# Performance work log

Measured on AMD Instinct MI355X. Metric: run time of the kernel, lower is better.

Reference implementation:

```python
import jax, jax.numpy as jnp
import numpy as np
from math import sqrt

P = 1.0  # axis-aligned transform exponent (init arg p)
EPS = 1e-6


def setup_inputs() -> dict:
    key = jax.random.key(0)
    k1, k2, k3, k4 = jax.random.split(key, 4)
    B, L, S, H, E = 4, 2048, 2048, 8, 64
    return {
        "queries": jax.random.normal(k1, (B, L, H, E), dtype=jnp.float32),
        "keys": jax.random.normal(k2, (B, S, H, E), dtype=jnp.float32),
        "values": jax.random.normal(k3, (B, S, H, E), dtype=jnp.float32),
        "attn_mask": jnp.zeros((1, 1, 1, 1), dtype=bool),  # unused: mask_flag=False
        "directional_weights": jnp.ones((1, 1, 1, 1), dtype=jnp.float32),
        "dynamic_param": jax.random.normal(k4, (1,), dtype=jnp.float32),
    }


def _transform(x, directional_weights, dynamic_param):
    # axis_aligned_transformation: rescale by (1/std over seq dim)^p (unbiased std, like torch)
    std = jnp.std(x, axis=-2, keepdims=True, ddof=1)
    x = x * (1.0 / (std + EPS)) ** P
    # directional_reweighting then nonlinear_mapping
    x = x * directional_weights
    return jnp.tanh(x) * dynamic_param


def reference(queries, keys, values, attn_mask, directional_weights, dynamic_param):
    B, L, H, E = queries.shape
    scale = 1.0 / sqrt(E)
    qt = _transform(queries, directional_weights, dynamic_param)  # [B,L,H,E]
    kt = _transform(keys, directional_weights, dynamic_param)     # [B,S,H,E]
    scores = jnp.einsum('blhe,bshe->bhls', qt, kt)                # [B,H,L,S]
    # per-row tau = sqrt(var(scores) + eps), unbiased variance like torch.var
    tau = jnp.sqrt(jnp.var(scores, axis=-1, keepdims=True, ddof=1) + EPS)
    A = jax.nn.softmax(scale * scores / tau, axis=-1)             # [B,H,L,S]
    V = jnp.einsum('bhls,bshd->blhd', A, values)                  # [B,L,H,D]
    return V
```

## Files before the change

kernel.cpp:

```cpp
#include <hip/hip_runtime.h>
#include <math.h>

#define B_ 4
#define L_ 2048
#define S_ 2048
#define H_ 8
#define E_ 64
#define BH_ (B_*H_)
#define EPS 1e-6f
#define LOG2E 1.44269504088896340736f

typedef __attribute__((ext_vector_type(8))) short short8;
typedef __attribute__((ext_vector_type(4))) float f32x4;

__device__ __forceinline__ unsigned short f2bf(float f) {
    unsigned int u = __float_as_uint(f);
    u = (u + 0x7fffu + ((u >> 16) & 1u)) >> 16;
    return (unsigned short)u;
}

__device__ __forceinline__ float bf2f(unsigned short u) {
    return __uint_as_float(((unsigned int)u) << 16);
}

__device__ __forceinline__ float fast_tanh(float x) {
    float e = __expf(2.0f * x);
    return 1.0f - 2.0f / (e + 1.0f);
}

__device__ __forceinline__ unsigned int cvt_pk_bf16(float lo, float hi) {
    unsigned int r;
    asm("v_cvt_pk_bf16_f32 %0, %1, %2" : "=v"(r) : "v"(lo), "v"(hi));
    return r;
}
__device__ __forceinline__ float exp2_fast(float x) {
    float r;
    asm("v_exp_f32 %0, %1" : "=v"(r) : "v"(x));
    return r;
}
__device__ __forceinline__ void swap32(unsigned int &a, unsigned int &b) {
    asm("v_permlane32_swap_b32 %0, %1" : "+v"(a), "+v"(b));
}
__device__ __forceinline__ void swap16(unsigned int &a, unsigned int &b) {
    asm("v_permlane16_swap_b32 %0, %1" : "+v"(a), "+v"(b));
}

__global__ __launch_bounds__(256) void pre_kernel(
    const float* __restrict__ xq, const float* __restrict__ xk,
    const float* __restrict__ xv,
    unsigned short* __restrict__ qt, unsigned short* __restrict__ kt,
    unsigned short* __restrict__ vt, float* __restrict__ Gf,
    const float* __restrict__ dwp, const float* __restrict__ dpp)
{
    __shared__ float ls[64][65];
    int bx = blockIdx.x;
    int tid = threadIdx.x;
    if (bx < 4096) {
        const float* x = (bx < 2048) ? xq : xk;
        unsigned short* xt = (bx < 2048) ? qt : kt;
        int wv = tid >> 6, ln = tid & 63;
        int bl = (bx & 2047) * 4 + wv;
        int b = bl >> 11, l = bl & 2047;
        const float* xb = x + (size_t)bl * 512;
        float4 fa = *(const float4*)(xb + ln * 4);
        float4 fb = *(const float4*)(xb + 256 + ln * 4);
        float s0 = fa.x + fb.x, s1 = fa.y + fb.y, s2 = fa.z + fb.z, s3 = fa.w + fb.w;
        float q0 = fa.x * fa.x + fb.x * fb.x, q1 = fa.y * fa.y + fb.y * fb.y;
        float q2 = fa.z * fa.z + fb.z * fb.z, q3 = fa.w * fa.w + fb.w * fb.w;
        s0 += __shfl_xor(s0, 16); s1 += __shfl_xor(s1, 16);
        s2 += __shfl_xor(s2, 16); s3 += __shfl_xor(s3, 16);
        q0 += __shfl_xor(q0, 16); q1 += __shfl_xor(q1, 16);
        q2 += __shfl_xor(q2, 16); q3 += __shfl_xor(q3, 16);
        s0 += __shfl_xor(s0, 32); s1 += __shfl_xor(s1, 32);
        s2 += __shfl_xor(s2, 32); s3 += __shfl_xor(s3, 32);
        q0 += __shfl_xor(q0, 32); q1 += __shfl_xor(q1, 32);
        q2 += __shfl_xor(q2, 32); q3 += __shfl_xor(q3, 32);
        float dw = dwp[0], d = dpp[0];
        auto mkw = [&](float s, float q) {
            float mean = s * 0.125f;
            float var = (q - s * mean) * (1.f / 7.f);
            var = fmaxf(var, 0.f);
            return dw / (sqrtf(var) + EPS);
        };
        float w0 = mkw(s0, q0), w1 = mkw(s1, q1), w2 = mkw(s2, q2), w3 = mkw(s3, q3);
        float ta0 = fast_tanh(fa.x * w0) * d, ta1 = fast_tanh(fa.y * w1) * d;
        float ta2 = fast_tanh(fa.z * w2) * d, ta3 = fast_tanh(fa.w * w3) * d;
        float tb0 = fast_tanh(fb.x * w0) * d, tb1 = fast_tanh(fb.y * w1) * d;
        float tb2 = fast_tanh(fb.z * w2) * d, tb3 = fast_tanh(fb.w * w3) * d;
        uint2 pa, pb;
        pa.x = cvt_pk_bf16(ta0, ta1); pa.y = cvt_pk_bf16(ta2, ta3);
        pb.x = cvt_pk_bf16(tb0, tb1); pb.y = cvt_pk_bf16(tb2, tb3);
        int hh = ln >> 4, e0 = (ln & 15) * 4;
        *(uint2*)(xt + ((size_t)(b * 8 + hh) * 2048 + l) * 64 + e0) = pa;
        *(uint2*)(xt + ((size_t)(b * 8 + hh + 4) * 2048 + l) * 64 + e0) = pb;
    } else if (bx < 5120) {
        int t2 = bx - 4096;
        int s0 = (t2 & 31) * 64;
        int h = (t2 >> 5) & 7, b = t2 >> 8;
        int t = tid;
#pragma unroll
        for (int i = 0; i < 4; ++i) {
            int idx = t + i * 256;
            int r = idx >> 4, c4 = (idx & 15) * 4;
            const float4 f = *(const float4*)&xv[((size_t)(b * S_ + s0 + r) * H_ + h) * E_ + c4];
            ls[r][c4] = f.x; ls[r][c4 + 1] = f.y; ls[r][c4 + 2] = f.z; ls[r][c4 + 3] = f.w;
        }
        __syncthreads();
        size_t ob = ((size_t)(b * H_ + h) * (S_ / 64) + (s0 >> 6)) * 4096;
#pragma unroll
        for (int i = 0; i < 2; ++i) {
            int ri = t + i * 256;
            int et = ri >> 7, c = (ri >> 6) & 1, quad = (ri >> 4) & 3, m = ri & 15;
            int e = et * 16 + m, sb = c * 32 + quad * 8;
            uint4 u;
            u.x = cvt_pk_bf16(ls[sb + 0][e], ls[sb + 1][e]);
            u.y = cvt_pk_bf16(ls[sb + 2][e], ls[sb + 3][e]);
            u.z = cvt_pk_bf16(ls[sb + 4][e], ls[sb + 5][e]);
            u.w = cvt_pk_bf16(ls[sb + 6][e], ls[sb + 7][e]);
            *(uint4*)&vt[ob + (size_t)ri * 8] = u;
        }
    } else {
        for (int i = (bx - 5120) * 256 + tid; i < 32 * 4096 + 32 * 64; i += 32 * 256)
            Gf[i] = 0.f;
    }
}

__global__ __launch_bounds__(256) void gram_kernel(
    unsigned short* __restrict__ kt, float* __restrict__ Gf,
    float* __restrict__ ksum)
{
    __shared__ unsigned short ks[128 * 72];
    __shared__ float gs[4096];
    int g2 = blockIdx.x;
    int bh = g2 >> 2, part = g2 & 3;
    unsigned short* base = kt + (size_t)bh * S_ * E_ + (size_t)part * 512 * E_;
    int tid = threadIdx.x, lane = tid & 63, w = tid >> 6;
    int m = lane & 15, quad = lane >> 4;

    f32x4 acc[4][4];
#pragma unroll
    for (int i = 0; i < 4; ++i)
#pragma unroll
        for (int j = 0; j < 4; ++j) acc[i][j] = (f32x4){0.f, 0.f, 0.f, 0.f};
    float ksp[4] = {0.f, 0.f, 0.f, 0.f};

    short8 stg[4];
#pragma unroll
    for (int i = 0; i < 4; ++i)
        stg[i] = *(const short8*)(base + (size_t)(tid + i * 256) * 8);

    for (int ch = 0; ch < 4; ++ch) {
        __syncthreads();
#pragma unroll
        for (int i = 0; i < 4; ++i) {
            int u = tid + i * 256;
            *(short8*)&ks[(u >> 3) * 72 + (u & 7) * 8] = stg[i];
        }
        __syncthreads();
        if (ch < 3) {
#pragma unroll
            for (int i = 0; i < 4; ++i)
                stg[i] = *(const short8*)(base + (size_t)(ch + 1) * 8192 + (tid + i * 256) * 8);
        }
#pragma unroll
        for (int tt = 0; tt < 2; ++tt)
#pragma unroll
            for (int i = 0; i < 2; ++i) {
                int u = tid + i * 256;
                int nt = u >> 7, cc = (u >> 6) & 1, ln2 = u & 63;
                int mm = ln2 & 15, qq = ln2 >> 4;
                short8 vv = *(const short8*)&ks[(tt * 64 + nt * 16 + mm) * 72 + cc * 32 + qq * 8];
                *(uint4*)&base[(size_t)(ch * 2 + tt) * 4096 + (size_t)u * 8] = *(uint4*)&vv;
            }
        int s0 = w * 32;
        short8 af[4];
#pragma unroll
        for (int i = 0; i < 4; ++i) {
            short8 a;
#pragma unroll
            for (int kk = 0; kk < 8; ++kk) {
                unsigned short uv = ks[(s0 + quad * 8 + kk) * 72 + i * 16 + m];
                a[kk] = (short)uv;
                ksp[i] += bf2f(uv);
            }
            af[i] = a;
        }
#pragma unroll
        for (int i = 0; i < 4; ++i)
#pragma unroll
            for (int j = 0; j < 4; ++j)
                acc[i][j] = __builtin_amdgcn_mfma_f32_16x16x32_bf16(af[i], af[j], acc[i][j], 0, 0, 0);
    }
#pragma unroll
    for (int i = 0; i < 4; ++i) {
        ksp[i] += __shfl_xor(ksp[i], 16);
        ksp[i] += __shfl_xor(ksp[i], 32);
    }
    if (lane < 16) {
#pragma unroll
        for (int i = 0; i < 4; ++i)
            atomicAdd(&ksum[bh * 64 + i * 16 + lane], ksp[i]);
    }
    for (int w2 = 0; w2 < 4; ++w2) {
        if (w == w2) {
#pragma unroll
            for (int i = 0; i < 4; ++i)
#pragma unroll
                for (int j = 0; j < 4; ++j)
#pragma unroll
                    for (int r = 0; r < 4; ++r) {
                        int idx = (i * 16 + quad * 4 + r) * 64 + j * 16 + m;
                        if (w2 == 0) gs[idx] = acc[i][j][r]; else gs[idx] += acc[i][j][r];
                    }
        }
        __syncthreads();
    }
#pragma unroll
    for (int ii = 0; ii < 16; ++ii) {
        int idx = tid + ii * 256;
        atomicAdd(&Gf[bh * 4096 + idx], gs[idx]);
    }
}

__global__ __launch_bounds__(256, 2) void attn_kernel(
    const unsigned short* __restrict__ qt,
    const unsigned short* __restrict__ ktf,
    const unsigned short* __restrict__ vt,
    const float* __restrict__ Gf,
    const float* __restrict__ ksum,
    float* __restrict__ out)
{
    __shared__ float2 ascr_s[4 * 32];
    const int tid = threadIdx.x;
    const int lane = tid & 63;
    const int w = tid >> 6;
    const int m = lane & 15;
    const int quad = lane >> 4;
    float2* ascr = ascr_s + w * 32;

    int blk = blockIdx.x;
    int bh = (blk & 7) * 4 + ((blk >> 3) & 3);
    int l0 = (blk >> 5) * 128;
    int b = bh >> 3, h = bh & 7;

    const unsigned short* qtb = qt + (size_t)bh * L_ * E_;
    const unsigned short* kb  = ktf + (size_t)bh * S_ * E_;
    const unsigned short* vtb = vt + (size_t)bh * (S_ / 64) * 4096;

    short8 qf[2][2];
#pragma unroll
    for (int g = 0; g < 2; ++g)
#pragma unroll
        for (int c = 0; c < 2; ++c)
            qf[g][c] = *(const short8*)(qtb + (size_t)(l0 + w * 32 + g * 16 + m) * E_ + c * 32 + quad * 8);

    float al2[2], nalm2[2];
    {
        const float* gb = Gf + (size_t)bh * 4096;
        short8 gfr[4][2];
#pragma unroll
        for (int j = 0; j < 4; ++j)
#pragma unroll
            for (int c = 0; c < 2; ++c) {
                const float* gp = gb + (size_t)(j * 16 + m) * 64 + c * 32 + quad * 8;
                float4 f0 = *(const float4*)gp;
                float4 f1 = *(const float4*)(gp + 4);
                uint4 u;
                u.x = cvt_pk_bf16(f0.x, f0.y); u.y = cvt_pk_bf16(f0.z, f0.w);
                u.z = cvt_pk_bf16(f1.x, f1.y); u.w = cvt_pk_bf16(f1.z, f1.w);
                gfr[j][c] = *(short8*)&u;
            }
        float ksl[4];
#pragma unroll
        for (int j = 0; j < 4; ++j) ksl[j] = ksum[bh * 64 + j * 16 + m];
#pragma unroll
        for (int g = 0; g < 2; ++g) {
            f32x4 accj[4];
#pragma unroll
            for (int j = 0; j < 4; ++j) {
                accj[j] = (f32x4){0.f, 0.f, 0.f, 0.f};
                accj[j] = __builtin_amdgcn_mfma_f32_16x16x32_bf16(qf[g][0], gfr[j][0], accj[j], 0, 0, 0);
                accj[j] = __builtin_amdgcn_mfma_f32_16x16x32_bf16(qf[g][1], gfr[j][1], accj[j], 0, 0, 0);
            }
            float ps[4] = {0, 0, 0, 0}, pr[4] = {0, 0, 0, 0};
#pragma unroll
            for (int r = 0; r < 4; ++r)
#pragma unroll
                for (int j = 0; j < 4; ++j) {
                    float qv = bf2f(qtb[(size_t)(l0 + w * 32 + g * 16 + quad * 4 + r) * E_ + j * 16 + m]);
                    ps[r] = fmaf(accj[j][r], qv, ps[r]);
                    pr[r] = fmaf(qv, ksl[j], pr[r]);
                }
#pragma unroll
            for (int mask = 1; mask < 16; mask <<= 1)
#pragma unroll
                for (int r = 0; r < 4; ++r) {
                    ps[r] += __shfl_xor(ps[r], mask);
                    pr[r] += __shfl_xor(pr[r], mask);
                }
            if (m == 0) {
#pragma unroll
                for (int r = 0; r < 4; ++r) {
                    float sum = pr[r];
                    float mu = sum * (1.f / S_);
                    float var = (ps[r] - sum * mu) * (1.f / (S_ - 1));
                    var = fmaxf(var, 0.f);
                    float tau = sqrtf(var + EPS);
                    float a = 0.125f / tau;
                    ascr[g * 16 + quad * 4 + r] = make_float2(a, a * mu);
                }
            }
        }
#pragma unroll
        for (int g = 0; g < 2; ++g) {
            float2 a2 = ascr[g * 16 + m];
            al2[g] = a2.x * LOG2E; nalm2[g] = -a2.y * LOG2E;
        }
    }

    f32x4 oacc[2][4];
#pragma unroll
    for (int g = 0; g < 2; ++g)
#pragma unroll
        for (int et = 0; et < 4; ++et) oacc[g][et] = (f32x4){0.f, 0.f, 0.f, 0.f};
    f32x4 asum2[2];
#pragma unroll
    for (int g = 0; g < 2; ++g) asum2[g] = (f32x4){0.f, 0.f, 0.f, 0.f};

    short8 ones;
#pragma unroll
    for (int j = 0; j < 8; ++j) ones[j] = (short)0x3F80;

#pragma unroll 2
    for (int st = 0; st < S_ / 64; ++st) {
        const unsigned short* kstb = kb + (size_t)st * 4096;
        const unsigned short* vstb = vtb + (size_t)st * 4096;
        short8 kf[4][2];
#pragma unroll
        for (int nt = 0; nt < 4; ++nt)
#pragma unroll
            for (int c = 0; c < 2; ++c)
                kf[nt][c] = *(const short8*)(kstb + (nt * 2 + c) * 512 + lane * 8);
        short8 vf[2][4];
#pragma unroll
        for (int c = 0; c < 2; ++c)
#pragma unroll
            for (int et = 0; et < 4; ++et)
                vf[c][et] = *(const short8*)(vstb + et * 1024 + c * 512 + lane * 8);

        unsigned int W[2][4][2];
#pragma unroll
        for (int nt = 0; nt < 4; ++nt)
#pragma unroll
            for (int g = 0; g < 2; ++g) {
                f32x4 acc = (f32x4){0.f, 0.f, 0.f, 0.f};
                acc = __builtin_amdgcn_mfma_f32_16x16x32_bf16(kf[nt][0], qf[g][0], acc, 0, 0, 0);
                acc = __builtin_amdgcn_mfma_f32_16x16x32_bf16(kf[nt][1], qf[g][1], acc, 0, 0, 0);
                float p0 = exp2_fast(fmaf(al2[g], acc[0], nalm2[g]));
                float p1 = exp2_fast(fmaf(al2[g], acc[1], nalm2[g]));
                float p2 = exp2_fast(fmaf(al2[g], acc[2], nalm2[g]));
                float p3 = exp2_fast(fmaf(al2[g], acc[3], nalm2[g]));
                W[g][nt][0] = cvt_pk_bf16(p0, p1);
                W[g][nt][1] = cvt_pk_bf16(p2, p3);
            }
#pragma unroll
        for (int g = 0; g < 2; ++g) {
            short8 pf[2];
#pragma unroll
            for (int c = 0; c < 2; ++c) {
                unsigned int a0 = W[g][2 * c][0], b0 = W[g][2 * c + 1][0];
                unsigned int a1 = W[g][2 * c][1], b1 = W[g][2 * c + 1][1];
                swap32(a0, b0); swap16(a0, b0);
                swap32(a1, b1); swap16(a1, b1);
                uint4 pk4;
                pk4.x = a0; pk4.y = a1; pk4.z = b0; pk4.w = b1;
                pf[c] = *(short8*)&pk4;
            }
#pragma unroll
            for (int et = 0; et < 4; ++et) {
                oacc[g][et] = __builtin_amdgcn_mfma_f32_16x16x32_bf16(pf[0], vf[0][et], oacc[g][et], 0, 0, 0);
                oacc[g][et] = __builtin_amdgcn_mfma_f32_16x16x32_bf16(pf[1], vf[1][et], oacc[g][et], 0, 0, 0);
            }
            asum2[g] = __builtin_amdgcn_mfma_f32_16x16x32_bf16(pf[0], ones, asum2[g], 0, 0, 0);
            asum2[g] = __builtin_amdgcn_mfma_f32_16x16x32_bf16(pf[1], ones, asum2[g], 0, 0, 0);
        }
    }

#pragma unroll
    for (int g = 0; g < 2; ++g)
#pragma unroll
        for (int r = 0; r < 4; ++r) {
            float rd = 1.0f / asum2[g][r];
            size_t row = (size_t)(b * L_ + l0 + w * 32 + g * 16 + quad * 4 + r);
#pragma unroll
            for (int et = 0; et < 4; ++et)
                out[(row * H_ + h) * E_ + et * 16 + m] = oacc[g][et][r] * rd;
        }
}

extern "C" void kernel_launch(void* const* d_in, const int* in_sizes, int n_in,
                              void* d_out, int out_size, void* d_ws, size_t ws_size,
                              hipStream_t stream)
{
    const float* q = (const float*)d_in[0];
    const float* k = (const float*)d_in[1];
    const float* v = (const float*)d_in[2];
    const float* dw = (const float*)d_in[4];
    const float* dp = (const float*)d_in[5];
    float* out = (float*)d_out;

    unsigned short* qt = (unsigned short*)d_ws;
    unsigned short* kt = qt + (size_t)BH_ * L_ * E_;
    unsigned short* vt = kt + (size_t)BH_ * S_ * E_;
    float* Gf = (float*)(vt + (size_t)BH_ * E_ * S_);
    float* ksum = Gf + (size_t)BH_ * 4096;

    pre_kernel<<<5152, 256, 0, stream>>>(q, k, v, qt, kt, vt, Gf, dw, dp);
    gram_kernel<<<128, 256, 0, stream>>>(kt, Gf, ksum);
    attn_kernel<<<512, 256, 0, stream>>>(qt, kt, vt, Gf, ksum, out);
}
```

Measured before the change: 154.0 us.

## Split attention key loop across two wave groups and combine partials in LDS

Doubles the attention block to 512 threads. Each group of four waves processes half of the S dimension for the same 128 query rows, and the second group passes its partial output and row sums through shared memory to the first group for the final normalization. The tau/mu statistics computation is also split by g between the two groups and synchronized via LDS. This doubles the waves in flight per CU to raise latency hiding, at the cost of an extra LDS reduction, two block barriers and a tighter register budget under launch_bounds(512,4).

Measured after the change: 243.3 us. +58.0%, slower.

```diff
diff --git a/kernel.cpp b/kernel.cpp
--- a/kernel.cpp
+++ b/kernel.cpp
@@ -222,7 +222,7 @@
     }
 }
 
-__global__ __launch_bounds__(256, 2) void attn_kernel(
+__global__ __launch_bounds__(512, 4) void attn_kernel(
     const unsigned short* __restrict__ qt,
     const unsigned short* __restrict__ ktf,
     const unsigned short* __restrict__ vt,
@@ -230,13 +230,16 @@
     const float* __restrict__ ksum,
     float* __restrict__ out)
 {
-    __shared__ float2 ascr_s[4 * 32];
+    __shared__ float comb[128][66];
+    __shared__ float dcomb[128];
+    __shared__ float2 ascr2[128];
     const int tid = threadIdx.x;
     const int lane = tid & 63;
     const int w = tid >> 6;
+    const int wr = w & 3;
+    const int sh = w >> 2;
     const int m = lane & 15;
     const int quad = lane >> 4;
-    float2* ascr = ascr_s + w * 32;
 
     int blk = blockIdx.x;
     int bh = (blk & 7) * 4 + ((blk >> 3) & 3);
@@ -252,7 +255,7 @@
     for (int g = 0; g < 2; ++g)
 #pragma unroll
         for (int c = 0; c < 2; ++c)
-            qf[g][c] = *(const short8*)(qtb + (size_t)(l0 + w * 32 + g * 16 + m) * E_ + c * 32 + quad * 8);
+            qf[g][c] = *(const short8*)(qtb + (size_t)(l0 + wr * 32 + g * 16 + m) * E_ + c * 32 + quad * 8);
 
     float al2[2], nalm2[2];
     {
@@ -273,48 +276,47 @@
         float ksl[4];
 #pragma unroll
         for (int j = 0; j < 4; ++j) ksl[j] = ksum[bh * 64 + j * 16 + m];
-#pragma unroll
-        for (int g = 0; g < 2; ++g) {
-            f32x4 accj[4];
+        const int g = sh;
+        f32x4 accj[4];
+#pragma unroll
+        for (int j = 0; j < 4; ++j) {
+            accj[j] = (f32x4){0.f, 0.f, 0.f, 0.f};
+            accj[j] = __builtin_amdgcn_mfma_f32_16x16x32_bf16(qf[g][0], gfr[j][0], accj[j], 0, 0, 0);
+            accj[j] = __builtin_amdgcn_mfma_f32_16x16x32_bf16(qf[g][1], gfr[j][1], accj[j], 0, 0, 0);
+        }
+        float ps[4] = {0, 0, 0, 0}, pr[4] = {0, 0, 0, 0};
+#pragma unroll
+        for (int r = 0; r < 4; ++r)
 #pragma unroll
             for (int j = 0; j < 4; ++j) {
-                accj[j] = (f32x4){0.f, 0.f, 0.f, 0.f};
-                accj[j] = __builtin_amdgcn_mfma_f32_16x16x32_bf16(qf[g][0], gfr[j][0], accj[j], 0, 0, 0);
-                accj[j] = __builtin_amdgcn_mfma_f32_16x16x32_bf16(qf[g][1], gfr[j][1], accj[j], 0, 0, 0);
-            }
-            float ps[4] = {0, 0, 0, 0}, pr[4] = {0, 0, 0, 0};
-#pragma unroll
-            for (int r = 0; r < 4; ++r)
-#pragma unroll
-                for (int j = 0; j < 4; ++j) {
-                    float qv = bf2f(qtb[(size_t)(l0 + w * 32 + g * 16 + quad * 4 + r) * E_ + j * 16 + m]);
-                    ps[r] = fmaf(accj[j][r], qv, ps[r]);
-                    pr[r] = fmaf(qv, ksl[j], pr[r]);
-                }
-#pragma unroll
-            for (int mask = 1; mask < 16; mask <<= 1)
-#pragma unroll
-                for (int r = 0; r < 4; ++r) {
-                    ps[r] += __shfl_xor(ps[r], mask);
-                    pr[r] += __shfl_xor(pr[r], mask);
-                }
-            if (m == 0) {
-#pragma unroll
-                for (int r = 0; r < 4; ++r) {
-                    float sum = pr[r];
-                    float mu = sum * (1.f / S_);
-                    float var = (ps[r] - sum * mu) * (1.f / (S_ - 1));
-                    var = fmaxf(var, 0.f);
-                    float tau = sqrtf(var + EPS);
-                    float a = 0.125f / tau;
-                    ascr[g * 16 + quad * 4 + r] = make_float2(a, a * mu);
-                }
-            }
-        }
-#pragma unroll
-        for (int g = 0; g < 2; ++g) {
-            float2 a2 = ascr[g * 16 + m];
-            al2[g] = a2.x * LOG2E; nalm2[g] = -a2.y * LOG2E;
+                float qv = bf2f(qtb[(size_t)(l0 + wr * 32 + g * 16 + quad * 4 + r) * E_ + j * 16 + m]);
+                ps[r] = fmaf(accj[j][r], qv, ps[r]);
+                pr[r] = fmaf(qv, ksl[j], pr[r]);
+            }
+#pragma unroll
+        for (int mask = 1; mask < 16; mask <<= 1)
+#pragma unroll
+            for (int r = 0; r < 4; ++r) {
+                ps[r] += __shfl_xor(ps[r], mask);
+                pr[r] += __shfl_xor(pr[r], mask);
+            }
+        if (m == 0) {
+#pragma unroll
+            for (int r = 0; r < 4; ++r) {
+                float sum = pr[r];
+                float mu = sum * (1.f / S_);
+                float var = (ps[r] - sum * mu) * (1.f / (S_ - 1));
+                var = fmaxf(var, 0.f);
+                float tau = sqrtf(var + EPS);
+                float a = 0.125f / tau;
+                ascr2[wr * 32 + g * 16 + quad * 4 + r] = make_float2(a, a * mu);
+            }
+        }
+        __syncthreads();
+#pragma unroll
+        for (int gg = 0; gg < 2; ++gg) {
+            float2 a2 = ascr2[wr * 32 + gg * 16 + m];
+            al2[gg] = a2.x * LOG2E; nalm2[gg] = -a2.y * LOG2E;
         }
     }
 
@@ -331,8 +333,10 @@
 #pragma unroll
     for (int j = 0; j < 8; ++j) ones[j] = (short)0x3F80;
 
+    const int st0 = sh * (S_ / 128);
 #pragma unroll 2
-    for (int st = 0; st < S_ / 64; ++st) {
+    for (int sti = 0; sti < S_ / 128; ++sti) {
+        int st = st0 + sti;
         const unsigned short* kstb = kb + (size_t)st * 4096;
         const unsigned short* vstb = vtb + (size_t)st * 4096;
         short8 kf[4][2];
@@ -386,16 +390,33 @@
         }
     }
 
-#pragma unroll
-    for (int g = 0; g < 2; ++g)
-#pragma unroll
-        for (int r = 0; r < 4; ++r) {
-            float rd = 1.0f / asum2[g][r];
-            size_t row = (size_t)(b * L_ + l0 + w * 32 + g * 16 + quad * 4 + r);
-#pragma unroll
-            for (int et = 0; et < 4; ++et)
-                out[(row * H_ + h) * E_ + et * 16 + m] = oacc[g][et][r] * rd;
-        }
+    if (sh == 1) {
+#pragma unroll
+        for (int g = 0; g < 2; ++g)
+#pragma unroll
+            for (int r = 0; r < 4; ++r) {
+                int row = wr * 32 + g * 16 + quad * 4 + r;
+                if (m == 0) dcomb[row] = asum2[g][r];
+#pragma unroll
+                for (int et = 0; et < 4; ++et)
+                    comb[row][et * 16 + m] = oacc[g][et][r];
+            }
+    }
+    __syncthreads();
+    if (sh == 0) {
+#pragma unroll
+        for (int g = 0; g < 2; ++g)
+#pragma unroll
+            for (int r = 0; r < 4; ++r) {
+                int row = wr * 32 + g * 16 + quad * 4 + r;
+                float rd = 1.0f / (asum2[g][r] + dcomb[row]);
+                size_t grow = (size_t)(b * L_ + l0 + row);
+#pragma unroll
+                for (int et = 0; et < 4; ++et)
+                    out[(grow * H_ + h) * E_ + et * 16 + m] =
+                        (oacc[g][et][r] + comb[row][et * 16 + m]) * rd;
+            }
+    }
 }
 
 extern "C" void kernel_launch(void* const* d_in, const int* in_sizes, int n_in,
@@ -417,5 +438,5 @@
 
     pre_kernel<<<5152, 256, 0, stream>>>(q, k, v, qt, kt, vt, Gf, dw, dp);
     gram_kernel<<<128, 256, 0, stream>>>(kt, Gf, ksum);
-    attn_kernel<<<512, 256, 0, stream>>>(qt, kt, vt, Gf, ksum, out);
-}
+    attn_kernel<<<512, 512, 0, stream>>>(qt, kt, vt, Gf, ksum, out);
+}
```
